# Optimization experiments

Measured on AMD Instinct MI355X. Metric: run time of the kernel, lower is better.

The kernel has to match this reference:

```python
import jax, jax.numpy as jnp
import numpy as np

N_NODES = 100000
N_EDGES = 3200000
IN_DIM = 128
H1, F1 = 8, 8          # layer1: 8 heads x 8 feats -> concat 64
N_CLASSES = 40         # layer2: 1 head -> classes
NEG_SLOPE = 0.2        # GAT LeakyReLU slope


def setup_inputs() -> dict:
    key = jax.random.key(0)
    ks = jax.random.split(key, 8)
    x = jax.random.normal(ks[0], (N_NODES, IN_DIM), dtype=jnp.float32)
    adj = jax.random.randint(ks[1], (2, N_EDGES), 0, N_NODES, dtype=jnp.int64)
    s1 = 1.0 / np.sqrt(IN_DIM)
    s2 = 1.0 / np.sqrt(H1 * F1)
    W1 = jax.random.normal(ks[2], (IN_DIM, H1 * F1), dtype=jnp.float32) * s1
    a1_src = jax.random.normal(ks[3], (H1, F1), dtype=jnp.float32) * s2
    a1_dst = jax.random.normal(ks[4], (H1, F1), dtype=jnp.float32) * s2
    W2 = jax.random.normal(ks[5], (H1 * F1, N_CLASSES), dtype=jnp.float32) * s2
    a2_src = jax.random.normal(ks[6], (1, N_CLASSES), dtype=jnp.float32) * s2
    a2_dst = jax.random.normal(ks[7], (1, N_CLASSES), dtype=jnp.float32) * s2
    return {"input_matrix": x, "adjacency_coo_matrix": adj,
            "W1": W1, "a1_src": a1_src, "a1_dst": a1_dst,
            "W2": W2, "a2_src": a2_src, "a2_dst": a2_dst}


def gat_layer(x, src, dst, W, a_s, a_d, heads, fdim):
    n = x.shape[0]
    h = (x @ W).reshape(n, heads, fdim)                 # [N,H,F]
    e_src = jnp.sum(h * a_s, axis=-1)                   # [N,H]
    e_dst = jnp.sum(h * a_d, axis=-1)                   # [N,H]
    e = jax.nn.leaky_relu(e_src[src] + e_dst[dst], NEG_SLOPE)  # [E,H]
    m = jax.ops.segment_max(e, dst, num_segments=n)     # per-dst softmax max
    p = jnp.exp(e - m[dst])
    s = jax.ops.segment_sum(p, dst, num_segments=n)
    alpha = p / s[dst]                                  # [E,H]
    out = jax.ops.segment_sum(alpha[:, :, None] * h[src], dst, num_segments=n)
    return out                                          # [N,H,F]


def reference(input_matrix, adjacency_coo_matrix, W1, a1_src, a1_dst, W2, a2_src, a2_dst):
    n = input_matrix.shape[0]
    loops = jnp.arange(n, dtype=adjacency_coo_matrix.dtype)
    src = jnp.concatenate([adjacency_coo_matrix[0], loops])
    dst = jnp.concatenate([adjacency_coo_matrix[1], loops])
    x = gat_layer(input_matrix, src, dst, W1, a1_src, a1_dst, H1, F1)
    x = jax.nn.elu(x.reshape(n, H1 * F1))               # concat heads + ELU
    x = gat_layer(x, src, dst, W2, a2_src, a2_dst, 1, N_CLASSES)
    return jax.nn.log_softmax(x.reshape(n, N_CLASSES), axis=1)
```

## Files before the change

### kernel.cpp

```cpp
#include <hip/hip_runtime.h>
#include <hip/hip_fp16.h>
#include <math.h>

#define NN 100000
#define EE 3200000
#define ET (EE + NN)
#define BKW 128
#define NBK ((NN + BKW - 1) / BKW)
#define BCAP 5120
#define EPB 4096
#define NB_P1 ((EE + EPB - 1) / EPB)
#define NB_G 391

typedef float v2f __attribute__((ext_vector_type(2)));
typedef float v4f __attribute__((ext_vector_type(4)));
typedef _Float16 v8h __attribute__((ext_vector_type(8)));

__device__ __forceinline__ float lrelu(float v) { return fmaxf(v, 0.2f * v); }

__device__ __forceinline__ unsigned char to_fp8(float v) {
  return (unsigned char)(__builtin_amdgcn_cvt_pk_fp8_f32(v, v, 0, false) & 0xff);
}


__global__ __launch_bounds__(256) void k_p1g1(
    const int* __restrict__ srcs, const int* __restrict__ dsts,
    int* __restrict__ bcount, int* __restrict__ bbuf,
    const float* __restrict__ x, const float* __restrict__ W1,
    const float* __restrict__ a1d,
    unsigned char* __restrict__ P1, float* __restrict__ ed1) {
  __shared__ char smem[16 * 64 * 8 * 2];
  int tid = threadIdx.x;
  if (blockIdx.x < NB_P1) {
    int* lcnt  = (int*)smem;
    int* lbase = lcnt + NBK;
    for (int i = tid; i < NBK; i += 256) lcnt[i] = 0;
    __syncthreads();
    int e0 = blockIdx.x * EPB;
    int rank[16], bkt[16], pk[16];
#pragma unroll
    for (int i = 0; i < 16; ++i) {
      int e = e0 + tid + i * 256;
      bkt[i] = -1;
      if (e < EE) {
        int d = dsts[e];
        int s = srcs[e];
        int b = d >> 7;
        rank[i] = atomicAdd(&lcnt[b], 1);
        bkt[i] = b;
        pk[i] = (s << 7) | (d & 127);
      }
    }
    __syncthreads();
    for (int i = tid; i < NBK; i += 256) {
      int c = lcnt[i];
      lbase[i] = c ? atomicAdd(&bcount[i], c) : 0;
    }
    __syncthreads();
#pragma unroll
    for (int i = 0; i < 16; ++i) {
      if (bkt[i] >= 0) {
        bbuf[(size_t)bkt[i] * BCAP + lbase[bkt[i]] + rank[i]] = pk[i];
      }
    }
    return;
  }
  _Float16* Wb = (_Float16*)smem;
  int gbid = blockIdx.x - NB_P1;
  for (int idx = tid; idx < 16 * 64; idx += 256) {
    int f = idx >> 6, l = idx & 63;
    int nt = f >> 2, kk = f & 3;
    int ql = l >> 4, cl = l & 15;
    int col = nt * 16 + cl;
    int k0 = kk * 32 + ql * 8;
    v8h tmp;
#pragma unroll
    for (int j = 0; j < 8; ++j) tmp[j] = (_Float16)W1[(k0 + j) * 64 + col];
    *reinterpret_cast<v8h*>(&Wb[idx * 8]) = tmp;
  }
  __syncthreads();
  int wv = tid >> 6, lane = tid & 63;
  int q = lane >> 4, c = lane & 15;
  v8h bf[16];
#pragma unroll
  for (int f = 0; f < 16; ++f)
    bf[f] = *reinterpret_cast<const v8h*>(&Wb[(f * 64 + lane) * 8]);
  float a1d_l[4];
#pragma unroll
  for (int nt = 0; nt < 4; ++nt) a1d_l[nt] = a1d[nt * 16 + c];
  for (int t = 0; t < 4; ++t) {
    int n0 = gbid * 256 + wv * 64 + t * 16;
    int row = n0 + c;
    row = (row < NN) ? row : (NN - 1);
    v4f acc[4] = {{0.f,0.f,0.f,0.f},{0.f,0.f,0.f,0.f},{0.f,0.f,0.f,0.f},{0.f,0.f,0.f,0.f}};
#pragma unroll
    for (int kk = 0; kk < 4; ++kk) {
      const float* xp = x + (size_t)row * 128 + kk * 32 + q * 8;
      float4 x0 = *reinterpret_cast<const float4*>(xp);
      float4 x1 = *reinterpret_cast<const float4*>(xp + 4);
      v8h af;
      af[0] = (_Float16)x0.x; af[1] = (_Float16)x0.y;
      af[2] = (_Float16)x0.z; af[3] = (_Float16)x0.w;
      af[4] = (_Float16)x1.x; af[5] = (_Float16)x1.y;
      af[6] = (_Float16)x1.z; af[7] = (_Float16)x1.w;
#pragma unroll
      for (int nt = 0; nt < 4; ++nt)
        acc[nt] = __builtin_amdgcn_mfma_f32_16x16x32_f16(af, bf[nt * 4 + kk], acc[nt], 0, 0, 0);
    }
#pragma unroll
    for (int nt = 0; nt < 4; ++nt) {
#pragma unroll
      for (int r = 0; r < 4; ++r) {
        float val = acc[nt][r];
        float vd = val * a1d_l[nt];
        vd += __shfl_xor(vd, 1); vd += __shfl_xor(vd, 2); vd += __shfl_xor(vd, 4);
        int node = n0 + q * 4 + r;
        if (node < NN) {
          P1[((size_t)node << 6) + nt * 16 + c] = to_fp8(val);
          if ((c & 7) == 0) ed1[node * 8 + 2 * nt + (c >> 3)] = vd;
        }
      }
    }
  }
}


__global__ __launch_bounds__(256) void k_p2(const int* __restrict__ bcount,
                                            const int* __restrict__ bbuf,
                                            int* __restrict__ offsets,
                                            int* __restrict__ edge_src) {
  __shared__ int cnt[BKW];
  __shared__ int s1[BKW];
  __shared__ int cur[BKW];
  __shared__ int red[256];
  int b = blockIdx.x, tid = threadIdx.x;
  int partial = 0;
  for (int j = tid; j < b; j += 256)
    partial += bcount[j] + min(BKW, NN - (j << 7));
  red[tid] = partial;
  __syncthreads();
  for (int off = 128; off >= 1; off >>= 1) {
    if (tid < off) red[tid] += red[tid + off];
    __syncthreads();
  }
  int base = red[0];
  int d0 = b << 7;
  int width = min(BKW, NN - d0);
  int n = bcount[b];
  const int* buf = bbuf + (size_t)b * BCAP;
  if (tid < BKW) cnt[tid] = (tid < width) ? 1 : 0;
  __syncthreads();
  for (int i = tid; i < n; i += 256) atomicAdd(&cnt[buf[i] & 127], 1);
  __syncthreads();
  if (tid < BKW) s1[tid] = cnt[tid];
  __syncthreads();
  for (int off = 1; off < BKW; off <<= 1) {
    int u = (tid < BKW && tid >= off) ? s1[tid - off] : 0;
    __syncthreads();
    if (tid < BKW) s1[tid] += u;
    __syncthreads();
  }
  if (tid < width) {
    int excl = s1[tid] - cnt[tid];
    offsets[d0 + tid] = base + excl;
    edge_src[base + excl] = d0 + tid;
    cur[tid] = excl + 1;
  }
  if (b == 0 && tid == 0) offsets[NN] = ET;
  __syncthreads();
  for (int i = tid; i < n; i += 256) {
    int p = buf[i];
    int pos = atomicAdd(&cur[p & 127], 1);
    edge_src[base + pos] = p >> 7;
  }
}


__global__ __launch_bounds__(256) void k_agg1(
    const int* __restrict__ offsets, const int* __restrict__ edge_src,
    const unsigned char* __restrict__ P1, const float* __restrict__ a1s,
    const float* __restrict__ ed1, __half* __restrict__ x2) {
  int wv = threadIdx.x >> 6, lane = threadIdx.x & 63;
  int g = lane >> 3, p = lane & 7;
  int dst = blockIdx.x * 32 + wv * 8 + g;
  float edv = ed1[dst * 8 + p];
  float4 as0 = *reinterpret_cast<const float4*>(a1s + p * 8);
  float4 as1 = *reinterpret_cast<const float4*>(a1s + p * 8 + 4);
  int beg = offsets[dst], end = offsets[dst + 1];
  int deg = end - beg;
  int md = deg;
#pragma unroll
  for (int o = 8; o < 64; o <<= 1) md = max(md, __shfl_xor(md, o, 64));
  float l = 0.f;
  float a[8] = {0.f, 0.f, 0.f, 0.f, 0.f, 0.f, 0.f, 0.f};
  for (int t = 0; t < md; t += 8) {
    int src[8]; uint2 raw[8];
#pragma unroll
    for (int i = 0; i < 8; ++i) {
      int idx = t + i;
      int ci = beg + ((idx < deg) ? idx : (deg - 1));
      src[i] = edge_src[ci];
    }
#pragma unroll
    for (int i = 0; i < 8; ++i)
      raw[i] = *reinterpret_cast<const uint2*>(P1 + ((size_t)src[i] << 6) + (p << 3));
#pragma unroll
    for (int i = 0; i < 8; ++i) {
      v2f f01 = __builtin_amdgcn_cvt_pk_f32_fp8(raw[i].x, false);
      v2f f23 = __builtin_amdgcn_cvt_pk_f32_fp8(raw[i].x, true);
      v2f f45 = __builtin_amdgcn_cvt_pk_f32_fp8(raw[i].y, false);
      v2f f67 = __builtin_amdgcn_cvt_pk_f32_fp8(raw[i].y, true);
      float es = f01.x * as0.x + f01.y * as0.y + f23.x * as0.z + f23.y * as0.w
               + f45.x * as1.x + f45.y * as1.y + f67.x * as1.z + f67.y * as1.w;
      float e = lrelu(es + edv);
      float pr = (t + i < deg) ? __expf(e) : 0.f;
      l += pr;
      a[0] += pr * f01.x; a[1] += pr * f01.y;
      a[2] += pr * f23.x; a[3] += pr * f23.y;
      a[4] += pr * f45.x; a[5] += pr * f45.y;
      a[6] += pr * f67.x; a[7] += pr * f67.y;
    }
  }
  float rl = 1.f / l;
  union { __half h[8]; uint4 u; } pk;
#pragma unroll
  for (int i = 0; i < 8; ++i) {
    float v = a[i] * rl;
    v = (v > 0.f) ? v : (__expf(v) - 1.f);
    pk.h[i] = __float2half(v);
  }
  *reinterpret_cast<uint4*>(x2 + ((size_t)dst << 6) + (p << 3)) = pk.u;
}


__global__ __launch_bounds__(256) void k_gemm2(
    const __half* __restrict__ x2, const float* __restrict__ W2,
    const float* __restrict__ a2s, const float* __restrict__ a2d,
    unsigned char* __restrict__ P2, float* __restrict__ ed2) {
  __shared__ _Float16 Wb[6 * 64 * 8];
  int tid = threadIdx.x;
  for (int idx = tid; idx < 6 * 64; idx += 256) {
    int f = idx >> 6, l = idx & 63;
    int nt = f >> 1, kk = f & 1;
    int ql = l >> 4, cl = l & 15;
    int col = nt * 16 + cl;
    int k0 = kk * 32 + ql * 8;
    v8h tmp;
#pragma unroll
    for (int j = 0; j < 8; ++j)
      tmp[j] = (col < 40) ? (_Float16)W2[(k0 + j) * 40 + col] : (_Float16)0.f;
    *reinterpret_cast<v8h*>(&Wb[idx * 8]) = tmp;
  }
  __syncthreads();
  int wv = tid >> 6, lane = tid & 63;
  int q = lane >> 4, c = lane & 15;
  v8h bf[6];
#pragma unroll
  for (int f = 0; f < 6; ++f)
    bf[f] = *reinterpret_cast<const v8h*>(&Wb[(f * 64 + lane) * 8]);
  float a2s_l[3], a2d_l[3];
#pragma unroll
  for (int nt = 0; nt < 3; ++nt) {
    int n = nt * 16 + c;
    a2s_l[nt] = (n < 40) ? a2s[n] : 0.f;
    a2d_l[nt] = (n < 40) ? a2d[n] : 0.f;
  }
  for (int t = 0; t < 4; ++t) {
    int n0 = blockIdx.x * 256 + wv * 64 + t * 16;
    int row = n0 + c;
    row = (row < NN) ? row : (NN - 1);
    v4f acc[3] = {{0.f,0.f,0.f,0.f},{0.f,0.f,0.f,0.f},{0.f,0.f,0.f,0.f}};
#pragma unroll
    for (int kk = 0; kk < 2; ++kk) {
      v8h af = *reinterpret_cast<const v8h*>(x2 + (size_t)row * 64 + kk * 32 + q * 8);
#pragma unroll
      for (int nt = 0; nt < 3; ++nt)
        acc[nt] = __builtin_amdgcn_mfma_f32_16x16x32_f16(af, bf[nt * 2 + kk], acc[nt], 0, 0, 0);
    }
#pragma unroll
    for (int r = 0; r < 4; ++r) {
      float v0 = acc[0][r], v1 = acc[1][r], v2 = acc[2][r];
      float s = v0 * a2s_l[0] + v1 * a2s_l[1] + v2 * a2s_l[2];
      float d = v0 * a2d_l[0] + v1 * a2d_l[1] + v2 * a2d_l[2];
      s += __shfl_xor(s, 1); s += __shfl_xor(s, 2); s += __shfl_xor(s, 4); s += __shfl_xor(s, 8);
      d += __shfl_xor(d, 1); d += __shfl_xor(d, 2); d += __shfl_xor(d, 4); d += __shfl_xor(d, 8);
      int node = n0 + q * 4 + r;
      if (node < NN) {
        unsigned char* rec = P2 + ((size_t)node << 6);
        if (c < 8) rec[32 + c] = to_fp8(v2);
        rec[c]      = to_fp8(v0);
        rec[16 + c] = to_fp8(v1);
        if (c == 0) {
          *reinterpret_cast<__half*>(rec + 40) = __float2half(s);
          ed2[node] = d;
        }
      }
    }
  }
}


__global__ __launch_bounds__(256) void k_agg2(
    const int* __restrict__ offsets, const int* __restrict__ edge_src,
    const unsigned char* __restrict__ P2, const float* __restrict__ ed2,
    float* __restrict__ out) {
  int wv = threadIdx.x >> 6, lane = threadIdx.x & 63;
  int g = lane >> 4, p = lane & 15;
  bool act = p < 10;
  int cp = act ? p : 0;
  int dst = blockIdx.x * 16 + wv * 4 + g;
  float edv = ed2[dst];
  int beg = offsets[dst], end = offsets[dst + 1];
  int deg = end - beg;
  int md = deg;
#pragma unroll
  for (int o = 16; o < 64; o <<= 1) md = max(md, __shfl_xor(md, o, 64));
  int gbase = lane & 48;
  int me = p & 7;
  float l = 0.f;
  float a[4] = {0.f, 0.f, 0.f, 0.f};
  for (int t = 0; t < md; t += 8) {
    int src[8]; unsigned raw[8];
#pragma unroll
    for (int i = 0; i < 8; ++i) {
      int ix = t + i;
      int ci = beg + ((ix < deg) ? ix : (deg - 1));
      src[i] = edge_src[ci];
    }
    float myes = __half2float(*reinterpret_cast<const __half*>(
        P2 + ((size_t)src[me] << 6) + 40));
    float mye = lrelu(myes + edv);
    float mypr = (t + me < deg) ? __expf(mye) : 0.f;
#pragma unroll
    for (int i = 0; i < 8; ++i)
      raw[i] = *reinterpret_cast<const unsigned*>(P2 + ((size_t)src[i] << 6) + (cp << 2));
#pragma unroll
    for (int i = 0; i < 8; ++i) {
      float pr = __shfl(mypr, gbase | i, 64);
      v2f f01 = __builtin_amdgcn_cvt_pk_f32_fp8(raw[i], false);
      v2f f23 = __builtin_amdgcn_cvt_pk_f32_fp8(raw[i], true);
      l += pr;
      a[0] += pr * f01.x; a[1] += pr * f01.y;
      a[2] += pr * f23.x; a[3] += pr * f23.y;
    }
  }
  float rl = 1.f / l;
  float v0 = a[0] * rl, v1 = a[1] * rl, v2 = a[2] * rl, v3 = a[3] * rl;
  float red = act ? fmaxf(fmaxf(v0, v1), fmaxf(v2, v3)) : -INFINITY;
#pragma unroll
  for (int o = 1; o < 16; o <<= 1) red = fmaxf(red, __shfl_xor(red, o, 64));
  float se = act ? (__expf(v0 - red) + __expf(v1 - red) + __expf(v2 - red) + __expf(v3 - red)) : 0.f;
#pragma unroll
  for (int o = 1; o < 16; o <<= 1) se += __shfl_xor(se, o, 64);
  float ls = red + __logf(se);
  if (act) {
    float4 o4 = make_float4(v0 - ls, v1 - ls, v2 - ls, v3 - ls);
    *reinterpret_cast<float4*>(out + (size_t)dst * 40 + (p << 2)) = o4;
  }
}


extern "C" void kernel_launch(void* const* d_in, const int* in_sizes, int n_in,
                              void* d_out, int out_size, void* d_ws, size_t ws_size,
                              hipStream_t stream) {
  const float* x   = (const float*)d_in[0];
  const int*   adj = (const int*)d_in[1];
  const float* W1  = (const float*)d_in[2];
  const float* a1s = (const float*)d_in[3];
  const float* a1d = (const float*)d_in[4];
  const float* W2  = (const float*)d_in[5];
  const float* a2s = (const float*)d_in[6];
  const float* a2d = (const float*)d_in[7];
  float* out = (float*)d_out;

  const int* srcs = adj;
  const int* dsts = adj + EE;

  char* w = (char*)d_ws;
  size_t off = 0;
  auto alloc = [&](size_t bytes) -> void* {
    void* p = w + off;
    off = (off + bytes + 255) & ~(size_t)255;
    return p;
  };
  int* offsets      = (int*)alloc((size_t)(NN + 1) * 4);
  int* edge_src     = (int*)alloc((size_t)ET * 4);
  int* bcount       = (int*)alloc((size_t)NBK * 4);
  unsigned char* P1 = (unsigned char*)alloc((size_t)NN * 64);
  float* ed1        = (float*)alloc((size_t)NN * 8 * 4);
  __half* x2        = (__half*)alloc((size_t)NN * 64 * 2);
  int* bbuf         = (int*)alloc((size_t)NBK * BCAP * 4);
  unsigned char* P2 = P1;
  float* ed2 = ed1;

  hipMemsetAsync(bcount, 0, (size_t)NBK * 4, stream);
  k_p1g1<<<NB_P1 + NB_G, 256, 0, stream>>>(srcs, dsts, bcount, bbuf,
                                           x, W1, a1d, P1, ed1);
  k_p2<<<NBK, 256, 0, stream>>>(bcount, bbuf, offsets, edge_src);

  k_agg1<<<NN / 32, 256, 0, stream>>>(offsets, edge_src, P1, a1s, ed1, x2);
  k_gemm2<<<NB_G, 256, 0, stream>>>(x2, W2, a2s, a2d, P2, ed2);
  k_agg2<<<NN / 16, 256, 0, stream>>>(offsets, edge_src, P2, ed2, out);
}
```

Baseline: 299.6 us.

## Split each node's edge list by source half to improve gather locality

The CSR build now partitions each destination's incoming edges into two runs, sources below 50000 and sources at or above it, and records the split point in a new mids array. Both aggregation kernels walk the two runs one after the other, so at any moment the waves in flight gather from roughly half of the P1/P2 feature table, which is meant to improve L2 hit rates on the random gathers. The cost is extra padding iterations, since each run is rounded up to 8 edges separately and lanes pad to the group maximum per run. The CSR kernel also does a 256-entry scan instead of a 128-entry one and writes one more array.

```diff
diff --git a/kernel.cpp b/kernel.cpp
--- a/kernel.cpp
+++ b/kernel.cpp
@@ -5,6 +5,7 @@
 #define NN 100000
 #define EE 3200000
 #define ET (EE + NN)
+#define HALF 50000
 #define BKW 128
 #define NBK ((NN + BKW - 1) / BKW)
 #define BCAP 5120
@@ -128,10 +129,11 @@
 __global__ __launch_bounds__(256) void k_p2(const int* __restrict__ bcount,
                                             const int* __restrict__ bbuf,
                                             int* __restrict__ offsets,
+                                            int* __restrict__ mids,
                                             int* __restrict__ edge_src) {
-  __shared__ int cnt[BKW];
-  __shared__ int s1[BKW];
-  __shared__ int cur[BKW];
+  __shared__ int cnt[256];
+  __shared__ int s1[256];
+  __shared__ int cur[256];
   __shared__ int red[256];
   int b = blockIdx.x, tid = threadIdx.x;
   int partial = 0;
@@ -148,36 +150,62 @@
   int width = min(BKW, NN - d0);
   int n = bcount[b];
   const int* buf = bbuf + (size_t)b * BCAP;
-  if (tid < BKW) cnt[tid] = (tid < width) ? 1 : 0;
-  __syncthreads();
-  for (int i = tid; i < n; i += 256) atomicAdd(&cnt[buf[i] & 127], 1);
-  __syncthreads();
-  if (tid < BKW) s1[tid] = cnt[tid];
-  __syncthreads();
-  for (int off = 1; off < BKW; off <<= 1) {
-    int u = (tid < BKW && tid >= off) ? s1[tid - off] : 0;
-    __syncthreads();
-    if (tid < BKW) s1[tid] += u;
-    __syncthreads();
-  }
-  if (tid < width) {
-    int excl = s1[tid] - cnt[tid];
-    offsets[d0 + tid] = base + excl;
-    edge_src[base + excl] = d0 + tid;
-    cur[tid] = excl + 1;
-  }
-  if (b == 0 && tid == 0) offsets[NN] = ET;
+  {
+    int ld = tid >> 1, hf = tid & 1;
+    int c = 0;
+    if (ld < width) {
+      int d = d0 + ld;
+      int sh = (d >= HALF) ? 1 : 0;
+      c = (sh == hf) ? 1 : 0;
+    }
+    cnt[tid] = c;
+  }
   __syncthreads();
   for (int i = tid; i < n; i += 256) {
     int p = buf[i];
-    int pos = atomicAdd(&cur[p & 127], 1);
-    edge_src[base + pos] = p >> 7;
+    int key = ((p & 127) << 1) | (((p >> 7) >= HALF) ? 1 : 0);
+    atomicAdd(&cnt[key], 1);
+  }
+  __syncthreads();
+  s1[tid] = cnt[tid];
+  __syncthreads();
+  for (int off = 1; off < 256; off <<= 1) {
+    int u = (tid >= off) ? s1[tid - off] : 0;
+    __syncthreads();
+    s1[tid] += u;
+    __syncthreads();
+  }
+  {
+    int ld = tid >> 1, hf = tid & 1;
+    if (ld < width) {
+      int excl = s1[tid] - cnt[tid];
+      int d = d0 + ld;
+      if (hf == 0) offsets[d] = base + excl;
+      else         mids[d]    = base + excl;
+      int sh = (d >= HALF) ? 1 : 0;
+      if (sh == hf) {
+        edge_src[base + excl] = d;
+        cur[tid] = excl + 1;
+      } else {
+        cur[tid] = excl;
+      }
+    }
+  }
+  if (b == 0 && tid == 0) offsets[NN] = ET;
+  __syncthreads();
+  for (int i = tid; i < n; i += 256) {
+    int p = buf[i];
+    int s = p >> 7;
+    int key = ((p & 127) << 1) | ((s >= HALF) ? 1 : 0);
+    int pos = atomicAdd(&cur[key], 1);
+    edge_src[base + pos] = s;
   }
 }
 
 
 __global__ __launch_bounds__(256) void k_agg1(
-    const int* __restrict__ offsets, const int* __restrict__ edge_src,
+    const int* __restrict__ offsets, const int* __restrict__ mids,
+    const int* __restrict__ edge_src,
     const unsigned char* __restrict__ P1, const float* __restrict__ a1s,
     const float* __restrict__ ed1, __half* __restrict__ x2) {
   int wv = threadIdx.x >> 6, lane = threadIdx.x & 63;
@@ -186,39 +214,43 @@
   float edv = ed1[dst * 8 + p];
   float4 as0 = *reinterpret_cast<const float4*>(a1s + p * 8);
   float4 as1 = *reinterpret_cast<const float4*>(a1s + p * 8 + 4);
-  int beg = offsets[dst], end = offsets[dst + 1];
-  int deg = end - beg;
-  int md = deg;
-#pragma unroll
-  for (int o = 8; o < 64; o <<= 1) md = max(md, __shfl_xor(md, o, 64));
+  int beg = offsets[dst], mid = mids[dst], end = offsets[dst + 1];
   float l = 0.f;
   float a[8] = {0.f, 0.f, 0.f, 0.f, 0.f, 0.f, 0.f, 0.f};
-  for (int t = 0; t < md; t += 8) {
-    int src[8]; uint2 raw[8];
-#pragma unroll
-    for (int i = 0; i < 8; ++i) {
-      int idx = t + i;
-      int ci = beg + ((idx < deg) ? idx : (deg - 1));
-      src[i] = edge_src[ci];
-    }
-#pragma unroll
-    for (int i = 0; i < 8; ++i)
-      raw[i] = *reinterpret_cast<const uint2*>(P1 + ((size_t)src[i] << 6) + (p << 3));
-#pragma unroll
-    for (int i = 0; i < 8; ++i) {
-      v2f f01 = __builtin_amdgcn_cvt_pk_f32_fp8(raw[i].x, false);
-      v2f f23 = __builtin_amdgcn_cvt_pk_f32_fp8(raw[i].x, true);
-      v2f f45 = __builtin_amdgcn_cvt_pk_f32_fp8(raw[i].y, false);
-      v2f f67 = __builtin_amdgcn_cvt_pk_f32_fp8(raw[i].y, true);
-      float es = f01.x * as0.x + f01.y * as0.y + f23.x * as0.z + f23.y * as0.w
-               + f45.x * as1.x + f45.y * as1.y + f67.x * as1.z + f67.y * as1.w;
-      float e = lrelu(es + edv);
-      float pr = (t + i < deg) ? __expf(e) : 0.f;
-      l += pr;
-      a[0] += pr * f01.x; a[1] += pr * f01.y;
-      a[2] += pr * f23.x; a[3] += pr * f23.y;
-      a[4] += pr * f45.x; a[5] += pr * f45.y;
-      a[6] += pr * f67.x; a[7] += pr * f67.y;
+#pragma unroll
+  for (int rg = 0; rg < 2; ++rg) {
+    int rb = rg ? mid : beg;
+    int dg = (rg ? end : mid) - rb;
+    int mdr = dg;
+#pragma unroll
+    for (int o = 8; o < 64; o <<= 1) mdr = max(mdr, __shfl_xor(mdr, o, 64));
+    for (int t = 0; t < mdr; t += 8) {
+      int src[8]; uint2 raw[8];
+#pragma unroll
+      for (int i = 0; i < 8; ++i) {
+        int idx = t + i;
+        int ci = (idx < dg) ? (rb + idx) : beg;
+        src[i] = edge_src[ci];
+      }
+#pragma unroll
+      for (int i = 0; i < 8; ++i)
+        raw[i] = *reinterpret_cast<const uint2*>(P1 + ((size_t)src[i] << 6) + (p << 3));
+#pragma unroll
+      for (int i = 0; i < 8; ++i) {
+        v2f f01 = __builtin_amdgcn_cvt_pk_f32_fp8(raw[i].x, false);
+        v2f f23 = __builtin_amdgcn_cvt_pk_f32_fp8(raw[i].x, true);
+        v2f f45 = __builtin_amdgcn_cvt_pk_f32_fp8(raw[i].y, false);
+        v2f f67 = __builtin_amdgcn_cvt_pk_f32_fp8(raw[i].y, true);
+        float es = f01.x * as0.x + f01.y * as0.y + f23.x * as0.z + f23.y * as0.w
+                 + f45.x * as1.x + f45.y * as1.y + f67.x * as1.z + f67.y * as1.w;
+        float e = lrelu(es + edv);
+        float pr = (t + i < dg) ? __expf(e) : 0.f;
+        l += pr;
+        a[0] += pr * f01.x; a[1] += pr * f01.y;
+        a[2] += pr * f23.x; a[3] += pr * f23.y;
+        a[4] += pr * f45.x; a[5] += pr * f45.y;
+        a[6] += pr * f67.x; a[7] += pr * f67.y;
+      }
     }
   }
   float rl = 1.f / l;
@@ -301,7 +333,8 @@
 
 
 __global__ __launch_bounds__(256) void k_agg2(
-    const int* __restrict__ offsets, const int* __restrict__ edge_src,
+    const int* __restrict__ offsets, const int* __restrict__ mids,
+    const int* __restrict__ edge_src,
     const unsigned char* __restrict__ P2, const float* __restrict__ ed2,
     float* __restrict__ out) {
   int wv = threadIdx.x >> 6, lane = threadIdx.x & 63;
@@ -310,38 +343,42 @@
   int cp = act ? p : 0;
   int dst = blockIdx.x * 16 + wv * 4 + g;
   float edv = ed2[dst];
-  int beg = offsets[dst], end = offsets[dst + 1];
-  int deg = end - beg;
-  int md = deg;
-#pragma unroll
-  for (int o = 16; o < 64; o <<= 1) md = max(md, __shfl_xor(md, o, 64));
+  int beg = offsets[dst], mid = mids[dst], end = offsets[dst + 1];
   int gbase = lane & 48;
   int me = p & 7;
   float l = 0.f;
   float a[4] = {0.f, 0.f, 0.f, 0.f};
-  for (int t = 0; t < md; t += 8) {
-    int src[8]; unsigned raw[8];
-#pragma unroll
-    for (int i = 0; i < 8; ++i) {
-      int ix = t + i;
-      int ci = beg + ((ix < deg) ? ix : (deg - 1));
-      src[i] = edge_src[ci];
-    }
-    float myes = __half2float(*reinterpret_cast<const __half*>(
-        P2 + ((size_t)src[me] << 6) + 40));
-    float mye = lrelu(myes + edv);
-    float mypr = (t + me < deg) ? __expf(mye) : 0.f;
-#pragma unroll
-    for (int i = 0; i < 8; ++i)
-      raw[i] = *reinterpret_cast<const unsigned*>(P2 + ((size_t)src[i] << 6) + (cp << 2));
-#pragma unroll
-    for (int i = 0; i < 8; ++i) {
-      float pr = __shfl(mypr, gbase | i, 64);
-      v2f f01 = __builtin_amdgcn_cvt_pk_f32_fp8(raw[i], false);
-      v2f f23 = __builtin_amdgcn_cvt_pk_f32_fp8(raw[i], true);
-      l += pr;
-      a[0] += pr * f01.x; a[1] += pr * f01.y;
-      a[2] += pr * f23.x; a[3] += pr * f23.y;
+#pragma unroll
+  for (int rg = 0; rg < 2; ++rg) {
+    int rb = rg ? mid : beg;
+    int dg = (rg ? end : mid) - rb;
+    int mdr = dg;
+#pragma unroll
+    for (int o = 16; o < 64; o <<= 1) mdr = max(mdr, __shfl_xor(mdr, o, 64));
+    for (int t = 0; t < mdr; t += 8) {
+      int src[8]; unsigned raw[8];
+#pragma unroll
+      for (int i = 0; i < 8; ++i) {
+        int ix = t + i;
+        int ci = (ix < dg) ? (rb + ix) : beg;
+        src[i] = edge_src[ci];
+      }
+      float myes = __half2float(*reinterpret_cast<const __half*>(
+          P2 + ((size_t)src[me] << 6) + 40));
+      float mye = lrelu(myes + edv);
+      float mypr = (t + me < dg) ? __expf(mye) : 0.f;
+#pragma unroll
+      for (int i = 0; i < 8; ++i)
+        raw[i] = *reinterpret_cast<const unsigned*>(P2 + ((size_t)src[i] << 6) + (cp << 2));
+#pragma unroll
+      for (int i = 0; i < 8; ++i) {
+        float pr = __shfl(mypr, gbase | i, 64);
+        v2f f01 = __builtin_amdgcn_cvt_pk_f32_fp8(raw[i], false);
+        v2f f23 = __builtin_amdgcn_cvt_pk_f32_fp8(raw[i], true);
+        l += pr;
+        a[0] += pr * f01.x; a[1] += pr * f01.y;
+        a[2] += pr * f23.x; a[3] += pr * f23.y;
+      }
     }
   }
   float rl = 1.f / l;
@@ -384,6 +421,7 @@
     return p;
   };
   int* offsets      = (int*)alloc((size_t)(NN + 1) * 4);
+  int* mids         = (int*)alloc((size_t)NN * 4);
   int* edge_src     = (int*)alloc((size_t)ET * 4);
   int* bcount       = (int*)alloc((size_t)NBK * 4);
   unsigned char* P1 = (unsigned char*)alloc((size_t)NN * 64);
@@ -396,9 +434,9 @@
   hipMemsetAsync(bcount, 0, (size_t)NBK * 4, stream);
   k_p1g1<<<NB_P1 + NB_G, 256, 0, stream>>>(srcs, dsts, bcount, bbuf,
                                            x, W1, a1d, P1, ed1);
-  k_p2<<<NBK, 256, 0, stream>>>(bcount, bbuf, offsets, edge_src);
-
-  k_agg1<<<NN / 32, 256, 0, stream>>>(offsets, edge_src, P1, a1s, ed1, x2);
+  k_p2<<<NBK, 256, 0, stream>>>(bcount, bbuf, offsets, mids, edge_src);
+
+  k_agg1<<<NN / 32, 256, 0, stream>>>(offsets, mids, edge_src, P1, a1s, ed1, x2);
   k_gemm2<<<NB_G, 256, 0, stream>>>(x2, W2, a2s, a2d, P2, ed2);
-  k_agg2<<<NN / 16, 256, 0, stream>>>(offsets, edge_src, P2, ed2, out);
-}
+  k_agg2<<<NN / 16, 256, 0, stream>>>(offsets, mids, edge_src, P2, ed2, out);
+}
```

Result: slower. 309.2 us (+3.2%).
